# Optimization experiments

Measured on AMD Instinct MI355X. Metric: run time of the kernel, lower is better.

Reference implementation:

```python
import jax, jax.numpy as jnp
import numpy as np

N_SRC = 200000
N_EDGES = 1280000
N_SEG = 100000
D = 64


def setup_inputs() -> dict:
    key = jax.random.key(0)
    k1, k2, k3 = jax.random.split(key, 3)
    values = jax.random.normal(k1, (N_SRC, D), dtype=jnp.float32)
    gather_idx = jax.random.randint(k2, (N_EDGES,), 0, N_SRC, dtype=jnp.int64)
    segment_ids = jnp.sort(jax.random.randint(k3, (N_EDGES,), 0, N_SEG, dtype=jnp.int64))
    return {
        "values": values,
        "gather_idx": gather_idx,
        "segment_ids": segment_ids,
        "num_segments": N_SEG,
    }


def reference(values, gather_idx, segment_ids, num_segments):
    # AGG_GATHER: indexed gather of input values  -> [E, D]
    gathered = values[gather_idx]
    # AGG_SCATTER_REDUCE: scatter_mean over ragged segments (sorted ids)
    sums = jax.ops.segment_sum(gathered, segment_ids, num_segments=num_segments,
                               indices_are_sorted=True)
    counts = jax.ops.segment_sum(jnp.ones((gathered.shape[0],), dtype=values.dtype),
                                 segment_ids, num_segments=num_segments,
                                 indices_are_sorted=True)
    # mean = sum / count (guard empty segments)
    return sums / jnp.maximum(counts, 1.0)[:, None]
```

## Files before the change

### kernel.cpp

```cpp
#include <hip/hip_runtime.h>


#define D 64

__global__ __launch_bounds__(256) void seg_starts_kernel(
    const int* __restrict__ segment_ids,
    int*       __restrict__ starts,
    int n_edges, int n_seg)
{
    const int e = blockIdx.x * blockDim.x + threadIdx.x;
    if (e >= n_edges) return;
    const int s     = segment_ids[e];
    const int sprev = (e == 0) ? -1 : segment_ids[e - 1];
    for (int t = sprev + 1; t <= s; ++t) starts[t] = e;
    if (e == n_edges - 1) {
        for (int t = s + 1; t <= n_seg; ++t) starts[t] = n_edges;
    }
}

__global__ __launch_bounds__(256) void seg_mean_kernel(
    const float* __restrict__ values,
    const int*   __restrict__ gather_idx,
    const int*   __restrict__ starts,
    float*       __restrict__ out,
    int n_seg)
{
    const int wave = (blockIdx.x * blockDim.x + threadIdx.x) >> 6;
    const int lane = threadIdx.x & 63;
    if (wave >= n_seg) return;

    const int start = starts[wave];
    const int end   = starts[wave + 1];

    float sum = 0.0f;
    int e = start;
    for (; e + 4 <= end; e += 4) {
        const int i0 = gather_idx[e + 0];
        const int i1 = gather_idx[e + 1];
        const int i2 = gather_idx[e + 2];
        const int i3 = gather_idx[e + 3];
        const float v0 = values[(i0 << 6) + lane];
        const float v1 = values[(i1 << 6) + lane];
        const float v2 = values[(i2 << 6) + lane];
        const float v3 = values[(i3 << 6) + lane];
        sum += (v0 + v1) + (v2 + v3);
    }
    for (; e < end; ++e)
        sum += values[(gather_idx[e] << 6) + lane];

    const int count = end - start;
    const float inv = (count > 0) ? (1.0f / (float)count) : 1.0f;
    out[(wave << 6) + lane] = sum * inv;
}

__global__ __launch_bounds__(256) void seg_mean_bsearch_kernel(
    const float* __restrict__ values,
    const int*   __restrict__ gather_idx,
    const int*   __restrict__ segment_ids,
    float*       __restrict__ out,
    int n_edges, int n_seg)
{
    const int wave = (blockIdx.x * blockDim.x + threadIdx.x) >> 6;
    const int lane = threadIdx.x & 63;
    if (wave >= n_seg) return;
    const int s = wave;
    int lo = 0, hi = n_edges;
    while (lo < hi) { int mid = (lo + hi) >> 1; if (segment_ids[mid] < s) lo = mid + 1; else hi = mid; }
    const int start = lo;
    hi = n_edges;
    while (lo < hi) { int mid = (lo + hi) >> 1; if (segment_ids[mid] < s + 1) lo = mid + 1; else hi = mid; }
    const int end = lo;
    float sum = 0.0f;
    for (int e = start; e < end; ++e) sum += values[(gather_idx[e] << 6) + lane];
    const int count = end - start;
    const float inv = (count > 0) ? (1.0f / (float)count) : 1.0f;
    out[(s << 6) + lane] = sum * inv;
}

extern "C" void kernel_launch(void* const* d_in, const int* in_sizes, int n_in,
                              void* d_out, int out_size, void* d_ws, size_t ws_size,
                              hipStream_t stream) {
    const float* values      = (const float*)d_in[0];
    const int*   gather_idx  = (const int*)d_in[1];
    const int*   segment_ids = (const int*)d_in[2];
    float* out = (float*)d_out;

    const int n_edges = in_sizes[1];
    const int n_seg   = out_size / D;

    const size_t starts_bytes = (size_t)(n_seg + 1) * sizeof(int);
    if (ws_size >= starts_bytes) {
        int* starts = (int*)d_ws;
        {
            const int threads = 256;
            const int blocks  = (n_edges + threads - 1) / threads;
            seg_starts_kernel<<<blocks, threads, 0, stream>>>(
                segment_ids, starts, n_edges, n_seg);
        }
        {
            const int threads = 256;
            const int blocks  = (n_seg * 64 + threads - 1) / threads;
            seg_mean_kernel<<<blocks, threads, 0, stream>>>(
                values, gather_idx, starts, out, n_seg);
        }
    } else {
        const int threads = 256;
        const int blocks  = (n_seg * 64 + threads - 1) / threads;
        seg_mean_bsearch_kernel<<<blocks, threads, 0, stream>>>(
            values, gather_idx, segment_ids, out, n_edges, n_seg);
    }
}
```

Measured before the change: 156.8 us.

## Vectorize segment-mean gathers with float4 across four edge subgroups per wave

Restructures the per-segment wave so each 16-lane subgroup loads a full 256-byte row with float4 loads, letting a wave fetch 4 different edges per load instruction (16 edges per loop iteration) instead of one edge per scalar load. Partial sums are combined with cross-subgroup shuffles and only one subgroup writes the float4 output. The starts kernel reuses the neighbor's segment id via a wave shuffle instead of a second global load, and index math is widened to 64-bit. This trades extra masking work and wasted loads on short segments (average ~13 edges) for fewer, wider memory transactions and more loads in flight per wave.

```diff
diff --git a/kernel.cpp b/kernel.cpp
--- a/kernel.cpp
+++ b/kernel.cpp
@@ -8,13 +8,18 @@
     int*       __restrict__ starts,
     int n_edges, int n_seg)
 {
-    const int e = blockIdx.x * blockDim.x + threadIdx.x;
-    if (e >= n_edges) return;
-    const int s     = segment_ids[e];
-    const int sprev = (e == 0) ? -1 : segment_ids[e - 1];
-    for (int t = sprev + 1; t <= s; ++t) starts[t] = e;
-    if (e == n_edges - 1) {
-        for (int t = s + 1; t <= n_seg; ++t) starts[t] = n_edges;
+    const int e      = blockIdx.x * blockDim.x + threadIdx.x;
+    const bool active = (e < n_edges);
+    const int ec     = active ? e : (n_edges - 1);
+    const int s      = segment_ids[ec];
+    const int lane   = threadIdx.x & 63;
+    int sprev        = __shfl_up(s, 1, 64);
+    if (lane == 0) sprev = (ec == 0) ? -1 : segment_ids[ec - 1];
+    if (active) {
+        for (int t = sprev + 1; t <= s; ++t) starts[t] = e;
+        if (e == n_edges - 1) {
+            for (int t = s + 1; t <= n_seg; ++t) starts[t] = n_edges;
+        }
     }
 }
 
@@ -29,28 +34,59 @@
     const int lane = threadIdx.x & 63;
     if (wave >= n_seg) return;
 
+    const int sub = lane >> 4;
+    const int cg  = lane & 15;
+
     const int start = starts[wave];
     const int end   = starts[wave + 1];
 
-    float sum = 0.0f;
-    int e = start;
-    for (; e + 4 <= end; e += 4) {
-        const int i0 = gather_idx[e + 0];
-        const int i1 = gather_idx[e + 1];
-        const int i2 = gather_idx[e + 2];
-        const int i3 = gather_idx[e + 3];
-        const float v0 = values[(i0 << 6) + lane];
-        const float v1 = values[(i1 << 6) + lane];
-        const float v2 = values[(i2 << 6) + lane];
-        const float v3 = values[(i3 << 6) + lane];
-        sum += (v0 + v1) + (v2 + v3);
+    float4 acc = make_float4(0.f, 0.f, 0.f, 0.f);
+
+    for (int base = start; base < end; base += 16) {
+        const int e0 = base + 0  + sub;
+        const int e1 = base + 4  + sub;
+        const int e2 = base + 8  + sub;
+        const int e3 = base + 12 + sub;
+        const bool m0 = e0 < end;
+        const bool m1 = e1 < end;
+        const bool m2 = e2 < end;
+        const bool m3 = e3 < end;
+        const int i0 = gather_idx[m0 ? e0 : start];
+        const int i1 = gather_idx[m1 ? e1 : start];
+        const int i2 = gather_idx[m2 ? e2 : start];
+        const int i3 = gather_idx[m3 ? e3 : start];
+        const float4 v0 = *(const float4*)(values + ((long long)i0 << 6) + (cg << 2));
+        const float4 v1 = *(const float4*)(values + ((long long)i1 << 6) + (cg << 2));
+        const float4 v2 = *(const float4*)(values + ((long long)i2 << 6) + (cg << 2));
+        const float4 v3 = *(const float4*)(values + ((long long)i3 << 6) + (cg << 2));
+        acc.x += m0 ? v0.x : 0.f; acc.y += m0 ? v0.y : 0.f;
+        acc.z += m0 ? v0.z : 0.f; acc.w += m0 ? v0.w : 0.f;
+        acc.x += m1 ? v1.x : 0.f; acc.y += m1 ? v1.y : 0.f;
+        acc.z += m1 ? v1.z : 0.f; acc.w += m1 ? v1.w : 0.f;
+        acc.x += m2 ? v2.x : 0.f; acc.y += m2 ? v2.y : 0.f;
+        acc.z += m2 ? v2.z : 0.f; acc.w += m2 ? v2.w : 0.f;
+        acc.x += m3 ? v3.x : 0.f; acc.y += m3 ? v3.y : 0.f;
+        acc.z += m3 ? v3.z : 0.f; acc.w += m3 ? v3.w : 0.f;
     }
-    for (; e < end; ++e)
-        sum += values[(gather_idx[e] << 6) + lane];
+
+    acc.x += __shfl_xor(acc.x, 16, 64);
+    acc.y += __shfl_xor(acc.y, 16, 64);
+    acc.z += __shfl_xor(acc.z, 16, 64);
+    acc.w += __shfl_xor(acc.w, 16, 64);
+    acc.x += __shfl_xor(acc.x, 32, 64);
+    acc.y += __shfl_xor(acc.y, 32, 64);
+    acc.z += __shfl_xor(acc.z, 32, 64);
+    acc.w += __shfl_xor(acc.w, 32, 64);
 
     const int count = end - start;
     const float inv = (count > 0) ? (1.0f / (float)count) : 1.0f;
-    out[(wave << 6) + lane] = sum * inv;
+
+    if (sub == 0) {
+        float4 r;
+        r.x = acc.x * inv; r.y = acc.y * inv;
+        r.z = acc.z * inv; r.w = acc.w * inv;
+        *(float4*)(out + ((long long)wave << 6) + (cg << 2)) = r;
+    }
 }
 
 __global__ __launch_bounds__(256) void seg_mean_bsearch_kernel(
@@ -71,10 +107,10 @@
     while (lo < hi) { int mid = (lo + hi) >> 1; if (segment_ids[mid] < s + 1) lo = mid + 1; else hi = mid; }
     const int end = lo;
     float sum = 0.0f;
-    for (int e = start; e < end; ++e) sum += values[(gather_idx[e] << 6) + lane];
+    for (int e = start; e < end; ++e) sum += values[((long long)gather_idx[e] << 6) + lane];
     const int count = end - start;
     const float inv = (count > 0) ? (1.0f / (float)count) : 1.0f;
-    out[(s << 6) + lane] = sum * inv;
+    out[((long long)s << 6) + lane] = sum * inv;
 }
 
 extern "C" void kernel_launch(void* const* d_in, const int* in_sizes, int n_in,
```

New measurement: 138.1 us. 11.9% less time.
